# Performance work log

Hardware: AMD Instinct MI355X
Metric: run time of the kernel (lower is better)

Reference implementation:

```python
import jax, jax.numpy as jnp
import numpy as np

V, D, H, L, S, B, FF, MAXLEN = 50257, 768, 12, 12, 1024, 4, 3072, 1024
HD = D // H
EPS = 1e-5


def layernorm(x, w, b):
    m = jnp.mean(x, axis=-1, keepdims=True)
    v = jnp.mean(jnp.square(x - m), axis=-1, keepdims=True)
    return (x - m) * jax.lax.rsqrt(v + EPS) * w + b


def setup_inputs() -> dict:
    key = jax.random.key(0)
    ks = jax.random.split(key, 8)
    std = 0.02
    return {
        "tokens": jax.random.randint(ks[0], (B, S), 0, V, dtype=jnp.int32),
        "wte": std * jax.random.normal(ks[1], (V, D), jnp.float32),
        "wpe": std * jax.random.normal(ks[2], (1, MAXLEN, D), jnp.float32),
        "ln1_w": jnp.ones((L, D), jnp.float32),
        "ln1_b": jnp.zeros((L, D), jnp.float32),
        "ln2_w": jnp.ones((L, D), jnp.float32),
        "ln2_b": jnp.zeros((L, D), jnp.float32),
        "W_exp": std * jax.random.normal(ks[3], (L, D, 3 * D), jnp.float32),
        "b_exp": jnp.zeros((L, 3 * D), jnp.float32),
        "W_o": std * jax.random.normal(ks[4], (L, D, D), jnp.float32),
        "b_o": jnp.zeros((L, D), jnp.float32),
        "W_ff1": std * jax.random.normal(ks[5], (L, D, FF), jnp.float32),
        "b_ff1": jnp.zeros((L, FF), jnp.float32),
        "W_ff2": std * jax.random.normal(ks[6], (L, FF, D), jnp.float32),
        "b_ff2": jnp.zeros((L, D), jnp.float32),
    }


def reference(tokens, wte, wpe, ln1_w, ln1_b, ln2_w, ln2_b,
              W_exp, b_exp, W_o, b_o, W_ff1, b_ff1, W_ff2, b_ff2):
    Bc, Sc = tokens.shape
    x = wte[tokens] + wpe[:, :Sc, :]                      # [B,S,D]
    mask = jnp.tril(jnp.ones((Sc, Sc), bool))             # causal (past=None)
    scale = 1.0 / jnp.sqrt(jnp.float32(HD))
    presents = []
    for l in range(L):
        h = layernorm(x, ln1_w[l], ln1_b[l])
        qkv = h @ W_exp[l] + b_exp[l]                     # [B,S,3D]
        q, k, v = jnp.split(qkv, 3, axis=-1)
        q = q.reshape(Bc, Sc, H, HD)
        k = k.reshape(Bc, Sc, H, HD)
        v = v.reshape(Bc, Sc, H, HD)
        presents.append(jnp.stack([k, v]))                # [2,B,S,H,HD]
        score = jnp.einsum('bqhd,bkhd->bhqk', q, k)
        score = jnp.where(mask, score, jnp.float32(-1e20))
        attn = jax.nn.softmax(score * scale, axis=-1)     # mask applied BEFORE scaling, as in source
        a = jnp.einsum('bhqk,bkhd->bqhd', attn, v).reshape(Bc, Sc, D)
        a = a @ W_o[l] + b_o[l]
        add = layernorm(a + x, ln2_w[l], ln2_b[l])        # LN2 on residual sum (GPT2-variant in source)
        ff = jax.nn.gelu(add @ W_ff1[l] + b_ff1[l], approximate=False)
        ff = ff @ W_ff2[l] + b_ff2[l]
        x = ff + add
    return x, jnp.stack(presents)                         # [L,2,B,S,H,HD]
```

## Files before the change

### kernel.cpp

```cpp
#include <hip/hip_runtime.h>
#include <hip/hip_bf16.h>
#include <math.h>

#define Bc 4
#define Sc 1024
#define Dc 768
#define Hc 12
#define Lc 12
#define FFc 3072
#define Mtot (Bc*Sc)

typedef __bf16 bf16x8 __attribute__((ext_vector_type(8)));
typedef float f32x4 __attribute__((ext_vector_type(4)));

__device__ __forceinline__ void gload_lds16(const void* g, void* l) {
    __builtin_amdgcn_global_load_lds((const __attribute__((address_space(1))) void*)g,
                                     (__attribute__((address_space(3))) void*)l, 16, 0, 0);
}

template <int N>
__device__ __forceinline__ void waitcnt_vm() {
    if constexpr (N == 0)       asm volatile("s_waitcnt vmcnt(0)" ::: "memory");
    else if constexpr (N == 4)  asm volatile("s_waitcnt vmcnt(4)" ::: "memory");
    else if constexpr (N == 5)  asm volatile("s_waitcnt vmcnt(5)" ::: "memory");
    else if constexpr (N == 8)  asm volatile("s_waitcnt vmcnt(8)" ::: "memory");
    else if constexpr (N == 10) asm volatile("s_waitcnt vmcnt(10)" ::: "memory");
    else static_assert(N == 0, "unsupported vmcnt");
}

__global__ __launch_bounds__(256) void embed_kernel(const int* __restrict__ tokens,
                                                    const float* __restrict__ wte,
                                                    const float* __restrict__ wpe,
                                                    float* __restrict__ x) {
    int row = blockIdx.x;
    int s = row & (Sc - 1);
    int tok = tokens[row];
    const float* wt = wte + (size_t)tok * Dc;
    const float* wp = wpe + (size_t)s * Dc;
    float* xr = x + (size_t)row * Dc;
#pragma unroll
    for (int k = 0; k < 3; ++k) {
        int d = threadIdx.x + k * 256;
        xr[d] = wt[d] + wp[d];
    }
}

__global__ __launch_bounds__(256) void prep_kernel(
        const float* __restrict__ We, const float* __restrict__ Wo,
        const float* __restrict__ Wf1, const float* __restrict__ Wf2,
        __bf16* __restrict__ Te, __bf16* __restrict__ To,
        __bf16* __restrict__ Tf1, __bf16* __restrict__ Tf2,
        const float* __restrict__ x, const float* __restrict__ lw,
        const float* __restrict__ lb, __bf16* __restrict__ outb) {
    __shared__ float shm[32 * 33];
    int bid = blockIdx.x;
    if (bid < 6912) {
        const float* W; __bf16* T; int K, N, t;
        if (bid < 1728)      { W = We;  T = Te;  K = 768;  N = 2304; t = bid; }
        else if (bid < 2304) { W = Wo;  T = To;  K = 768;  N = 768;  t = bid - 1728; }
        else if (bid < 4608) { W = Wf1; T = Tf1; K = 768;  N = 3072; t = bid - 2304; }
        else                 { W = Wf2; T = Tf2; K = 3072; N = 768;  t = bid - 4608; }
        int nx = N >> 5;
        int n0 = (t % nx) * 32, k0 = (t / nx) * 32;
        int tx = threadIdx.x & 31, ty = threadIdx.x >> 5;
#pragma unroll
        for (int i = 0; i < 4; ++i)
            shm[(ty + 8 * i) * 33 + tx] = W[(size_t)(k0 + ty + 8 * i) * N + n0 + tx];
        __syncthreads();
#pragma unroll
        for (int i = 0; i < 4; ++i)
            T[(size_t)(n0 + ty + 8 * i) * K + k0 + tx] = (__bf16)shm[tx * 33 + ty + 8 * i];
    } else {
        int row = bid - 6912;
        const float* xr = x + (size_t)row * Dc;
        int t = threadIdx.x;
        float v0 = xr[t], v1 = xr[t + 256], v2 = xr[t + 512];
        float s1 = v0 + v1 + v2;
        float s2 = v0 * v0 + v1 * v1 + v2 * v2;
#pragma unroll
        for (int o = 32; o; o >>= 1) {
            s1 += __shfl_down(s1, o);
            s2 += __shfl_down(s2, o);
        }
        int wv = t >> 6;
        if ((t & 63) == 0) { shm[wv] = s1; shm[4 + wv] = s2; }
        __syncthreads();
        float S1 = shm[0] + shm[1] + shm[2] + shm[3];
        float S2 = shm[4] + shm[5] + shm[6] + shm[7];
        float mean = S1 * (1.0f / Dc);
        float var = S2 * (1.0f / Dc) - mean * mean;
        float rs = rsqrtf(var + 1e-5f);
        size_t ro = (size_t)row * Dc;
        outb[ro + t]       = (__bf16)((v0 - mean) * rs * lw[t]       + lb[t]);
        outb[ro + t + 256] = (__bf16)((v1 - mean) * rs * lw[t + 256] + lb[t + 256]);
        outb[ro + t + 512] = (__bf16)((v2 - mean) * rs * lw[t + 512] + lb[t + 512]);
    }
}

__global__ __launch_bounds__(256) void ln_kernel(const float* __restrict__ x,
                                                 const float* __restrict__ lw,
                                                 const float* __restrict__ lb,
                                                 __bf16* __restrict__ outb,
                                                 float* __restrict__ outf) {
    int row = blockIdx.x;
    const float* xr = x + (size_t)row * Dc;
    int t = threadIdx.x;
    float v0 = xr[t], v1 = xr[t + 256], v2 = xr[t + 512];
    float s1 = v0 + v1 + v2;
    float s2 = v0 * v0 + v1 * v1 + v2 * v2;
    __shared__ float red[8];
#pragma unroll
    for (int o = 32; o; o >>= 1) {
        s1 += __shfl_down(s1, o);
        s2 += __shfl_down(s2, o);
    }
    int wv = t >> 6;
    if ((t & 63) == 0) { red[wv] = s1; red[4 + wv] = s2; }
    __syncthreads();
    float S1 = red[0] + red[1] + red[2] + red[3];
    float S2 = red[4] + red[5] + red[6] + red[7];
    float mean = S1 * (1.0f / Dc);
    float var = S2 * (1.0f / Dc) - mean * mean;
    float rs = rsqrtf(var + 1e-5f);
    size_t ro = (size_t)row * Dc;
    float o0 = (v0 - mean) * rs * lw[t]       + lb[t];
    float o1 = (v1 - mean) * rs * lw[t + 256] + lb[t + 256];
    float o2 = (v2 - mean) * rs * lw[t + 512] + lb[t + 512];
    outb[ro + t]       = (__bf16)o0;
    outb[ro + t + 256] = (__bf16)o1;
    outb[ro + t + 512] = (__bf16)o2;
    outf[ro + t]       = o0;
    outf[ro + t + 256] = o1;
    outf[ro + t + 512] = o2;
}

template <int BMr, int BNc, int BK, int EPI>
__global__ __launch_bounds__(256) void gemm_bf16(const __bf16* __restrict__ A,
                                                 const __bf16* __restrict__ BT,
                                                 const float* __restrict__ bias,
                                                 const float* __restrict__ addin,
                                                 float* __restrict__ Cf,
                                                 __bf16* __restrict__ Cb,
                                                 float* __restrict__ pres,
                                                 int K, int N) {
    constexpr int HRm = BMr / 32, HRn = BNc / 32;
    constexpr int KS  = BK / 32;
    constexpr int LPR = BK / 8;
    constexpr int SSH = (BK == 32) ? 1 : 0;
    constexpr int IA  = BMr * BK / 2048;
    constexpr int IB  = BNc * BK / 2048;
    constexpr int S1w = IA + IB;
    static_assert(IA * 2048 == BMr * BK && IB * 2048 == BNc * BK, "staging granularity");
    __shared__ __bf16 As[3][BMr * BK];
    __shared__ __bf16 Bs[3][BNc * BK];
    int tid = threadIdx.x;
    int w = tid >> 6, l = tid & 63;
    int wrow = (w >> 1) * (BMr / 2), wcol = (w & 1) * (BNc / 2);
    int brow0 = blockIdx.x * BMr, bcol0 = blockIdx.y * BNc;
    int rsel = l & 15, lg = l >> 4;

    f32x4 acc[HRm][HRn] = {};

    const __bf16* Abase = A + (size_t)brow0 * K;
    const __bf16* Bbase = BT + (size_t)bcol0 * K;

    auto stage = [&](int buf, int kt) {
#pragma unroll
        for (int i = 0; i < IA; ++i) {
            int cid = i * 256 + tid;
            int row = cid / LPR, slot = cid % LPR;
            int chunk = slot ^ ((row >> SSH) & (LPR - 1));
            gload_lds16(Abase + (size_t)row * K + kt + chunk * 8,
                        &As[buf][(i * 256 + w * 64) * 8]);
        }
#pragma unroll
        for (int i = 0; i < IB; ++i) {
            int cid = i * 256 + tid;
            int row = cid / LPR, slot = cid % LPR;
            int chunk = slot ^ ((row >> SSH) & (LPR - 1));
            gload_lds16(Bbase + (size_t)row * K + kt + chunk * 8,
                        &Bs[buf][(i * 256 + w * 64) * 8]);
        }
    };

    int nk = K / BK;
    stage(0, 0);
    stage(1, BK);
    int cur = 0;
    for (int kt = 0; kt < nk; ++kt) {
        if (kt + 2 < nk) {
            int b2 = cur + 2; if (b2 >= 3) b2 -= 3;
            stage(b2, (kt + 2) * BK);
            waitcnt_vm<2 * S1w>();
        } else if (kt + 1 < nk) {
            waitcnt_vm<S1w>();
        } else {
            waitcnt_vm<0>();
        }
        __builtin_amdgcn_s_barrier();
        __builtin_amdgcn_sched_barrier(0);

        bf16x8 af[KS][HRm], bfr[KS][HRn];
#pragma unroll
        for (int m = 0; m < HRm; ++m) {
            int r = wrow + m * 16 + rsel;
            int sw = (r >> SSH) & (LPR - 1);
#pragma unroll
            for (int s = 0; s < KS; ++s)
                af[s][m] = *(const bf16x8*)(&As[cur][r * BK + ((s * 4 + lg) ^ sw) * 8]);
        }
#pragma unroll
        for (int n = 0; n < HRn; ++n) {
            int r = wcol + n * 16 + rsel;
            int sw = (r >> SSH) & (LPR - 1);
#pragma unroll
            for (int s = 0; s < KS; ++s)
                bfr[s][n] = *(const bf16x8*)(&Bs[cur][r * BK + ((s * 4 + lg) ^ sw) * 8]);
        }
#pragma unroll
        for (int s = 0; s < KS; ++s)
#pragma unroll
            for (int m = 0; m < HRm; ++m)
#pragma unroll
                for (int n = 0; n < HRn; ++n)
                    acc[m][n] = __builtin_amdgcn_mfma_f32_16x16x32_bf16(af[s][m], bfr[s][n], acc[m][n], 0, 0, 0);

        __builtin_amdgcn_sched_barrier(0);
        __builtin_amdgcn_s_barrier();
        cur = (cur == 2) ? 0 : cur + 1;
    }

    int r4 = lg * 4, cc = rsel;
#pragma unroll
    for (int m = 0; m < HRm; ++m)
#pragma unroll
        for (int n = 0; n < HRn; ++n) {
            int col = bcol0 + wcol + n * 16 + cc;
            float bv = bias[col];
#pragma unroll
            for (int i = 0; i < 4; ++i) {
                int row = brow0 + wrow + m * 16 + r4 + i;
                float v = acc[m][n][i] + bv;
                if (EPI == 1) {
                    v += addin[(size_t)row * N + col];
                    Cf[(size_t)row * N + col] = v;
                }
                if (EPI == 2) {
                    float u = 0.7978845608f * (v + 0.044715f * v * v * v);
                    v = v / (1.0f + __expf(-2.0f * u));
                    Cb[(size_t)row * N + col] = (__bf16)v;
                }
                if (EPI == 3) {
                    Cb[(size_t)row * N + col] = (__bf16)v;
                    if (col >= 768) {
                        int kv = (col >= 1536) ? 1 : 0;
                        pres[((size_t)kv * Mtot + row) * Dc + (col - 768 - kv * 768)] = v;
                    }
                }
            }
        }
}

__global__ __launch_bounds__(256) void attn_mfma_kernel(const __bf16* __restrict__ qkvb,
                                                        __bf16* __restrict__ aout) {
    __shared__ __bf16 Ks[64 * 72];
    __shared__ __bf16 Vts[64 * 72];
    __shared__ __bf16 Ps[4][16 * 72];
    int bh = blockIdx.x;
    int b = bh / Hc, h = bh % Hc;
    int qt = (Sc / 64 - 1) - blockIdx.y;
    int tid = threadIdx.x;
    int w = tid >> 6, l = tid & 63;
    int lr = l & 15, lg = l >> 4;
    int qb = qt * 64;

    const __bf16* base = qkvb + (size_t)b * Sc * 2304 + h * 64;

    bf16x8 qf[2];
    {
        const __bf16* qrow = base + (size_t)(qb + w * 16 + lr) * 2304 + lg * 8;
        qf[0] = *(const bf16x8*)(qrow);
        qf[1] = *(const bf16x8*)(qrow + 32);
    }

    f32x4 O[4] = {};
    float mrow[4], lrowv[4];
#pragma unroll
    for (int i = 0; i < 4; ++i) { mrow[i] = -1e30f; lrowv[i] = 0.0f; }

    int kj = tid >> 2, kc = tid & 3;
    int vj = tid & 63, vd0 = (tid >> 6) * 8;

    for (int t = 0; t <= qt; ++t) {
        __syncthreads();
#pragma unroll
        for (int it = 0; it < 2; ++it) {
            int c = kc + 4 * it;
            bf16x8 v = *(const bf16x8*)(base + (size_t)(t * 64 + kj) * 2304 + 768 + c * 8);
            *(bf16x8*)(&Ks[kj * 72 + c * 8]) = v;
        }
#pragma unroll
        for (int it = 0; it < 2; ++it) {
            int d0 = vd0 + 32 * it;
            bf16x8 v = *(const bf16x8*)(base + (size_t)(t * 64 + vj) * 2304 + 1536 + d0);
#pragma unroll
            for (int i = 0; i < 8; ++i)
                Vts[(d0 + i) * 72 + vj] = v[i];
        }
        __syncthreads();

        f32x4 sc[4] = {};
        __builtin_amdgcn_s_setprio(1);
#pragma unroll
        for (int s = 0; s < 2; ++s)
#pragma unroll
            for (int n = 0; n < 4; ++n) {
                bf16x8 kf = *(const bf16x8*)(&Ks[(n * 16 + lr) * 72 + s * 32 + lg * 8]);
                sc[n] = __builtin_amdgcn_mfma_f32_16x16x32_bf16(qf[s], kf, sc[n], 0, 0, 0);
            }
        __builtin_amdgcn_s_setprio(0);

        bool diag = (t == qt);
#pragma unroll
        for (int n = 0; n < 4; ++n)
#pragma unroll
            for (int i = 0; i < 4; ++i) {
                float s = sc[n][i] * 0.125f;
                if (diag) {
                    int jg = n * 16 + lr;
                    int qg = w * 16 + lg * 4 + i;
                    if (jg > qg) s = -1e30f;
                }
                sc[n][i] = s;
            }
        float corr[4], psum[4];
#pragma unroll
        for (int i = 0; i < 4; ++i) {
            float mx = fmaxf(fmaxf(sc[0][i], sc[1][i]), fmaxf(sc[2][i], sc[3][i]));
#pragma unroll
            for (int o = 1; o < 16; o <<= 1) mx = fmaxf(mx, __shfl_xor(mx, o));
            float mnew = fmaxf(mrow[i], mx);
            corr[i] = __expf(mrow[i] - mnew);
            mrow[i] = mnew;
            psum[i] = 0.0f;
        }
#pragma unroll
        for (int n = 0; n < 4; ++n)
#pragma unroll
            for (int i = 0; i < 4; ++i) {
                float p = __expf(sc[n][i] - mrow[i]);
                psum[i] += p;
                Ps[w][(lg * 4 + i) * 72 + n * 16 + lr] = (__bf16)p;
            }
#pragma unroll
        for (int i = 0; i < 4; ++i) {
#pragma unroll
            for (int o = 1; o < 16; o <<= 1) psum[i] += __shfl_xor(psum[i], o);
            lrowv[i] = lrowv[i] * corr[i] + psum[i];
        }
#pragma unroll
        for (int n = 0; n < 4; ++n)
#pragma unroll
            for (int i = 0; i < 4; ++i) O[n][i] *= corr[i];
        __builtin_amdgcn_s_setprio(1);
#pragma unroll
        for (int s = 0; s < 2; ++s) {
            bf16x8 pf = *(const bf16x8*)(&Ps[w][lr * 72 + s * 32 + lg * 8]);
#pragma unroll
            for (int n = 0; n < 4; ++n) {
                bf16x8 vf = *(const bf16x8*)(&Vts[(n * 16 + lr) * 72 + s * 32 + lg * 8]);
                O[n] = __builtin_amdgcn_mfma_f32_16x16x32_bf16(pf, vf, O[n], 0, 0, 0);
            }
        }
        __builtin_amdgcn_s_setprio(0);
    }
    __bf16* orow = aout + (size_t)(b * Sc + qb + w * 16 + lg * 4) * Dc + h * 64 + lr;
#pragma unroll
    for (int n = 0; n < 4; ++n)
#pragma unroll
        for (int i = 0; i < 4; ++i)
            orow[(size_t)i * Dc + n * 16] = (__bf16)(O[n][i] / lrowv[i]);
}

extern "C" void kernel_launch(void* const* d_in, const int* in_sizes, int n_in,
                              void* d_out, int out_size, void* d_ws, size_t ws_size,
                              hipStream_t stream) {
    const int*   tokens = (const int*)d_in[0];
    const float* wte    = (const float*)d_in[1];
    const float* wpe    = (const float*)d_in[2];
    const float* ln1_w  = (const float*)d_in[3];
    const float* ln1_b  = (const float*)d_in[4];
    const float* ln2_w  = (const float*)d_in[5];
    const float* ln2_b  = (const float*)d_in[6];
    const float* W_exp  = (const float*)d_in[7];
    const float* b_exp  = (const float*)d_in[8];
    const float* W_o    = (const float*)d_in[9];
    const float* b_o    = (const float*)d_in[10];
    const float* W_ff1  = (const float*)d_in[11];
    const float* b_ff1  = (const float*)d_in[12];
    const float* W_ff2  = (const float*)d_in[13];
    const float* b_ff2  = (const float*)d_in[14];

    float* out_x    = (float*)d_out;
    float* out_pres = out_x + (size_t)Mtot * Dc;

    float* ws   = (float*)d_ws;
    float* x    = ws;
    float* addf = x + (size_t)Mtot * Dc;
    __bf16* hb   = (__bf16*)(addf + (size_t)Mtot * Dc);
    __bf16* addb = hb + (size_t)Mtot * Dc;
    __bf16* qkvb = addb + (size_t)Mtot * Dc;
    __bf16* ff1b = qkvb + (size_t)Mtot * 3 * Dc;
    __bf16* wt_exp = ff1b + (size_t)Mtot * FFc;
    __bf16* wt_o   = wt_exp + (size_t)2304 * 768;
    __bf16* wt_ff1 = wt_o   + (size_t)768 * 768;
    __bf16* wt_ff2 = wt_ff1 + (size_t)3072 * 768;

    embed_kernel<<<Mtot, 256, 0, stream>>>(tokens, wte, wpe, x);

    for (int lidx = 0; lidx < Lc; ++lidx) {
        prep_kernel<<<6912 + Mtot, 256, 0, stream>>>(
            W_exp + (size_t)lidx * 768 * 2304, W_o + (size_t)lidx * 768 * 768,
            W_ff1 + (size_t)lidx * 768 * 3072, W_ff2 + (size_t)lidx * 3072 * 768,
            wt_exp, wt_o, wt_ff1, wt_ff2,
            x, ln1_w + lidx * Dc, ln1_b + lidx * Dc, hb);

        gemm_bf16<64, 192, 32, 3><<<dim3(Mtot / 64, 2304 / 192), 256, 0, stream>>>(
            hb, wt_exp, b_exp + (size_t)lidx * 3 * Dc,
            nullptr, nullptr, qkvb, out_pres + (size_t)lidx * 2 * Mtot * Dc, 768, 2304);
        attn_mfma_kernel<<<dim3(Bc * Hc, Sc / 64), 256, 0, stream>>>(qkvb, hb);
        gemm_bf16<64, 96, 64, 1><<<dim3(Mtot / 64, 768 / 96), 256, 0, stream>>>(
            hb, wt_o, b_o + (size_t)lidx * Dc,
            x, x, nullptr, nullptr, 768, 768);
        ln_kernel<<<Mtot, 256, 0, stream>>>(
            x, ln2_w + lidx * Dc, ln2_b + lidx * Dc, addb, addf);
        gemm_bf16<128, 128, 32, 2><<<dim3(Mtot / 128, FFc / 128), 256, 0, stream>>>(
            addb, wt_ff1, b_ff1 + (size_t)lidx * FFc,
            nullptr, nullptr, ff1b, nullptr, 768, FFc);
        float* ff2dst = (lidx == Lc - 1) ? out_x : x;
        gemm_bf16<64, 96, 64, 1><<<dim3(Mtot / 64, 768 / 96), 256, 0, stream>>>(
            ff1b, wt_ff2, b_ff2 + (size_t)lidx * Dc,
            addf, ff2dst, nullptr, nullptr, 3072, 768);
    }
}
```

Baseline: 2.032 ms.

## Split-K the two N=768 GEMMs and fold partial sums into LayerNorm kernels

The attention-output and FF2 GEMMs now run as two K halves over a z grid dimension. One half adds bias and the residual; the other writes raw partial sums to a scratch buffer. The following LayerNorm kernels (ln2 and the next layer's prep) add the two partials, and a finalize kernel does the same for the output. This doubles the block count of these small-N GEMMs to improve CU occupancy and uses double buffering there. The cost is an extra fp32 write and read of the partial activations per GEMM, plus one extra kernel.

```diff
diff --git a/kernel.cpp b/kernel.cpp
--- a/kernel.cpp
+++ b/kernel.cpp
@@ -45,13 +45,16 @@
     }
 }
 
+template <bool SUMIN>
 __global__ __launch_bounds__(256) void prep_kernel(
         const float* __restrict__ We, const float* __restrict__ Wo,
         const float* __restrict__ Wf1, const float* __restrict__ Wf2,
         __bf16* __restrict__ Te, __bf16* __restrict__ To,
         __bf16* __restrict__ Tf1, __bf16* __restrict__ Tf2,
-        const float* __restrict__ x, const float* __restrict__ lw,
-        const float* __restrict__ lb, __bf16* __restrict__ outb) {
+        const float* __restrict__ xin0, const float* __restrict__ xin1,
+        float* __restrict__ xout,
+        const float* __restrict__ lw, const float* __restrict__ lb,
+        __bf16* __restrict__ outb) {
     __shared__ float shm[32 * 33];
     int bid = blockIdx.x;
     if (bid < 6912) {
@@ -72,9 +75,17 @@
             T[(size_t)(n0 + ty + 8 * i) * K + k0 + tx] = (__bf16)shm[tx * 33 + ty + 8 * i];
     } else {
         int row = bid - 6912;
-        const float* xr = x + (size_t)row * Dc;
+        size_t ro = (size_t)row * Dc;
         int t = threadIdx.x;
-        float v0 = xr[t], v1 = xr[t + 256], v2 = xr[t + 512];
+        float v0, v1, v2;
+        if (SUMIN) {
+            v0 = xin0[ro + t]       + xin1[ro + t];
+            v1 = xin0[ro + t + 256] + xin1[ro + t + 256];
+            v2 = xin0[ro + t + 512] + xin1[ro + t + 512];
+            xout[ro + t] = v0; xout[ro + t + 256] = v1; xout[ro + t + 512] = v2;
+        } else {
+            v0 = xin0[ro + t]; v1 = xin0[ro + t + 256]; v2 = xin0[ro + t + 512];
+        }
         float s1 = v0 + v1 + v2;
         float s2 = v0 * v0 + v1 * v1 + v2 * v2;
 #pragma unroll
@@ -90,22 +101,24 @@
         float mean = S1 * (1.0f / Dc);
         float var = S2 * (1.0f / Dc) - mean * mean;
         float rs = rsqrtf(var + 1e-5f);
-        size_t ro = (size_t)row * Dc;
         outb[ro + t]       = (__bf16)((v0 - mean) * rs * lw[t]       + lb[t]);
         outb[ro + t + 256] = (__bf16)((v1 - mean) * rs * lw[t + 256] + lb[t + 256]);
         outb[ro + t + 512] = (__bf16)((v2 - mean) * rs * lw[t + 512] + lb[t + 512]);
     }
 }
 
-__global__ __launch_bounds__(256) void ln_kernel(const float* __restrict__ x,
-                                                 const float* __restrict__ lw,
-                                                 const float* __restrict__ lb,
-                                                 __bf16* __restrict__ outb,
-                                                 float* __restrict__ outf) {
+__global__ __launch_bounds__(256) void ln2_kernel(const float* __restrict__ xin0,
+                                                  const float* __restrict__ xin1,
+                                                  const float* __restrict__ lw,
+                                                  const float* __restrict__ lb,
+                                                  __bf16* __restrict__ outb,
+                                                  float* __restrict__ outf) {
     int row = blockIdx.x;
-    const float* xr = x + (size_t)row * Dc;
+    size_t ro = (size_t)row * Dc;
     int t = threadIdx.x;
-    float v0 = xr[t], v1 = xr[t + 256], v2 = xr[t + 512];
+    float v0 = xin0[ro + t]       + xin1[ro + t];
+    float v1 = xin0[ro + t + 256] + xin1[ro + t + 256];
+    float v2 = xin0[ro + t + 512] + xin1[ro + t + 512];
     float s1 = v0 + v1 + v2;
     float s2 = v0 * v0 + v1 * v1 + v2 * v2;
     __shared__ float red[8];
@@ -122,7 +135,6 @@
     float mean = S1 * (1.0f / Dc);
     float var = S2 * (1.0f / Dc) - mean * mean;
     float rs = rsqrtf(var + 1e-5f);
-    size_t ro = (size_t)row * Dc;
     float o0 = (v0 - mean) * rs * lw[t]       + lb[t];
     float o1 = (v1 - mean) * rs * lw[t + 256] + lb[t + 256];
     float o2 = (v2 - mean) * rs * lw[t + 512] + lb[t + 512];
@@ -134,15 +146,26 @@
     outf[ro + t + 512] = o2;
 }
 
-template <int BMr, int BNc, int BK, int EPI>
+__global__ __launch_bounds__(256) void finalize_kernel(const float* __restrict__ a,
+                                                       const float* __restrict__ b,
+                                                       float* __restrict__ out) {
+    size_t idx = ((size_t)blockIdx.x * 256 + threadIdx.x) * 4;
+    float4 va = *(const float4*)(a + idx);
+    float4 vb = *(const float4*)(b + idx);
+    float4 o = make_float4(va.x + vb.x, va.y + vb.y, va.z + vb.z, va.w + vb.w);
+    *(float4*)(out + idx) = o;
+}
+
+template <int BMr, int BNc, int BK, int EPI, int NBUF, bool SPLIT>
 __global__ __launch_bounds__(256) void gemm_bf16(const __bf16* __restrict__ A,
                                                  const __bf16* __restrict__ BT,
                                                  const float* __restrict__ bias,
                                                  const float* __restrict__ addin,
                                                  float* __restrict__ Cf,
+                                                 float* __restrict__ Cf2,
                                                  __bf16* __restrict__ Cb,
                                                  float* __restrict__ pres,
-                                                 int K, int N) {
+                                                 int K, int Kst, int N) {
     constexpr int HRm = BMr / 32, HRn = BNc / 32;
     constexpr int KS  = BK / 32;
     constexpr int LPR = BK / 8;
@@ -151,18 +174,19 @@
     constexpr int IB  = BNc * BK / 2048;
     constexpr int S1w = IA + IB;
     static_assert(IA * 2048 == BMr * BK && IB * 2048 == BNc * BK, "staging granularity");
-    __shared__ __bf16 As[3][BMr * BK];
-    __shared__ __bf16 Bs[3][BNc * BK];
+    __shared__ __bf16 As[NBUF][BMr * BK];
+    __shared__ __bf16 Bs[NBUF][BNc * BK];
     int tid = threadIdx.x;
     int w = tid >> 6, l = tid & 63;
     int wrow = (w >> 1) * (BMr / 2), wcol = (w & 1) * (BNc / 2);
     int brow0 = blockIdx.x * BMr, bcol0 = blockIdx.y * BNc;
+    int koff = SPLIT ? blockIdx.z * K : 0;
     int rsel = l & 15, lg = l >> 4;
 
     f32x4 acc[HRm][HRn] = {};
 
-    const __bf16* Abase = A + (size_t)brow0 * K;
-    const __bf16* Bbase = BT + (size_t)bcol0 * K;
+    const __bf16* Abase = A + (size_t)brow0 * Kst + koff;
+    const __bf16* Bbase = BT + (size_t)bcol0 * Kst + koff;
 
     auto stage = [&](int buf, int kt) {
 #pragma unroll
@@ -170,7 +194,7 @@
             int cid = i * 256 + tid;
             int row = cid / LPR, slot = cid % LPR;
             int chunk = slot ^ ((row >> SSH) & (LPR - 1));
-            gload_lds16(Abase + (size_t)row * K + kt + chunk * 8,
+            gload_lds16(Abase + (size_t)row * Kst + kt + chunk * 8,
                         &As[buf][(i * 256 + w * 64) * 8]);
         }
 #pragma unroll
@@ -178,24 +202,33 @@
             int cid = i * 256 + tid;
             int row = cid / LPR, slot = cid % LPR;
             int chunk = slot ^ ((row >> SSH) & (LPR - 1));
-            gload_lds16(Bbase + (size_t)row * K + kt + chunk * 8,
+            gload_lds16(Bbase + (size_t)row * Kst + kt + chunk * 8,
                         &Bs[buf][(i * 256 + w * 64) * 8]);
         }
     };
 
     int nk = K / BK;
     stage(0, 0);
-    stage(1, BK);
+    if (NBUF == 3) stage(1, BK);
     int cur = 0;
     for (int kt = 0; kt < nk; ++kt) {
-        if (kt + 2 < nk) {
-            int b2 = cur + 2; if (b2 >= 3) b2 -= 3;
-            stage(b2, (kt + 2) * BK);
-            waitcnt_vm<2 * S1w>();
-        } else if (kt + 1 < nk) {
-            waitcnt_vm<S1w>();
+        if (NBUF == 3) {
+            if (kt + 2 < nk) {
+                int b2 = cur + 2; if (b2 >= 3) b2 -= 3;
+                stage(b2, (kt + 2) * BK);
+                waitcnt_vm<2 * S1w>();
+            } else if (kt + 1 < nk) {
+                waitcnt_vm<S1w>();
+            } else {
+                waitcnt_vm<0>();
+            }
         } else {
-            waitcnt_vm<0>();
+            if (kt + 1 < nk) {
+                stage(cur ^ 1, (kt + 1) * BK);
+                waitcnt_vm<S1w>();
+            } else {
+                waitcnt_vm<0>();
+            }
         }
         __builtin_amdgcn_s_barrier();
         __builtin_amdgcn_sched_barrier(0);
@@ -227,20 +260,26 @@
 
         __builtin_amdgcn_sched_barrier(0);
         __builtin_amdgcn_s_barrier();
-        cur = (cur == 2) ? 0 : cur + 1;
+        if (NBUF == 3) { cur = (cur == 2) ? 0 : cur + 1; } else { cur ^= 1; }
     }
 
     int r4 = lg * 4, cc = rsel;
+    bool rawpart = SPLIT && (blockIdx.z == 1);
 #pragma unroll
     for (int m = 0; m < HRm; ++m)
 #pragma unroll
         for (int n = 0; n < HRn; ++n) {
             int col = bcol0 + wcol + n * 16 + cc;
-            float bv = bias[col];
+            float bv = rawpart ? 0.0f : bias[col];
 #pragma unroll
             for (int i = 0; i < 4; ++i) {
                 int row = brow0 + wrow + m * 16 + r4 + i;
-                float v = acc[m][n][i] + bv;
+                float v = acc[m][n][i];
+                if (rawpart) {
+                    Cf2[(size_t)row * N + col] = v;
+                    continue;
+                }
+                v += bv;
                 if (EPI == 1) {
                     v += addin[(size_t)row * N + col];
                     Cf[(size_t)row * N + col] = v;
@@ -407,7 +446,9 @@
     float* ws   = (float*)d_ws;
     float* x    = ws;
     float* addf = x + (size_t)Mtot * Dc;
-    __bf16* hb   = (__bf16*)(addf + (size_t)Mtot * Dc);
+    float* p1w  = addf + (size_t)Mtot * Dc;
+    float* q1   = p1w + (size_t)Mtot * Dc;
+    __bf16* hb   = (__bf16*)(q1 + (size_t)Mtot * Dc);
     __bf16* addb = hb + (size_t)Mtot * Dc;
     __bf16* qkvb = addb + (size_t)Mtot * Dc;
     __bf16* ff1b = qkvb + (size_t)Mtot * 3 * Dc;
@@ -419,27 +460,35 @@
     embed_kernel<<<Mtot, 256, 0, stream>>>(tokens, wte, wpe, x);
 
     for (int lidx = 0; lidx < Lc; ++lidx) {
-        prep_kernel<<<6912 + Mtot, 256, 0, stream>>>(
-            W_exp + (size_t)lidx * 768 * 2304, W_o + (size_t)lidx * 768 * 768,
-            W_ff1 + (size_t)lidx * 768 * 3072, W_ff2 + (size_t)lidx * 3072 * 768,
-            wt_exp, wt_o, wt_ff1, wt_ff2,
-            x, ln1_w + lidx * Dc, ln1_b + lidx * Dc, hb);
-
-        gemm_bf16<64, 192, 32, 3><<<dim3(Mtot / 64, 2304 / 192), 256, 0, stream>>>(
+        if (lidx == 0) {
+            prep_kernel<false><<<6912 + Mtot, 256, 0, stream>>>(
+                W_exp, W_o, W_ff1, W_ff2, wt_exp, wt_o, wt_ff1, wt_ff2,
+                x, nullptr, nullptr, ln1_w, ln1_b, hb);
+        } else {
+            prep_kernel<true><<<6912 + Mtot, 256, 0, stream>>>(
+                W_exp + (size_t)lidx * 768 * 2304, W_o + (size_t)lidx * 768 * 768,
+                W_ff1 + (size_t)lidx * 768 * 3072, W_ff2 + (size_t)lidx * 3072 * 768,
+                wt_exp, wt_o, wt_ff1, wt_ff2,
+                addf, q1, x, ln1_w + lidx * Dc, ln1_b + lidx * Dc, hb);
+        }
+
+        gemm_bf16<64, 192, 32, 3, 3, false><<<dim3(Mtot / 64, 2304 / 192), 256, 0, stream>>>(
             hb, wt_exp, b_exp + (size_t)lidx * 3 * Dc,
-            nullptr, nullptr, qkvb, out_pres + (size_t)lidx * 2 * Mtot * Dc, 768, 2304);
+            nullptr, nullptr, nullptr, qkvb,
+            out_pres + (size_t)lidx * 2 * Mtot * Dc, 768, 768, 2304);
         attn_mfma_kernel<<<dim3(Bc * Hc, Sc / 64), 256, 0, stream>>>(qkvb, hb);
-        gemm_bf16<64, 96, 64, 1><<<dim3(Mtot / 64, 768 / 96), 256, 0, stream>>>(
+        gemm_bf16<64, 96, 64, 1, 2, true><<<dim3(Mtot / 64, 768 / 96, 2), 256, 0, stream>>>(
             hb, wt_o, b_o + (size_t)lidx * Dc,
-            x, x, nullptr, nullptr, 768, 768);
-        ln_kernel<<<Mtot, 256, 0, stream>>>(
-            x, ln2_w + lidx * Dc, ln2_b + lidx * Dc, addb, addf);
-        gemm_bf16<128, 128, 32, 2><<<dim3(Mtot / 128, FFc / 128), 256, 0, stream>>>(
+            x, x, p1w, nullptr, nullptr, 384, 768, 768);
+        ln2_kernel<<<Mtot, 256, 0, stream>>>(
+            x, p1w, ln2_w + lidx * Dc, ln2_b + lidx * Dc, addb, addf);
+        gemm_bf16<128, 128, 32, 2, 3, false><<<dim3(Mtot / 128, FFc / 128), 256, 0, stream>>>(
             addb, wt_ff1, b_ff1 + (size_t)lidx * FFc,
-            nullptr, nullptr, ff1b, nullptr, 768, FFc);
-        float* ff2dst = (lidx == Lc - 1) ? out_x : x;
-        gemm_bf16<64, 96, 64, 1><<<dim3(Mtot / 64, 768 / 96), 256, 0, stream>>>(
+            nullptr, nullptr, nullptr, ff1b, nullptr, 768, 768, FFc);
+        gemm_bf16<64, 96, 64, 1, 2, true><<<dim3(Mtot / 64, 768 / 96, 2), 256, 0, stream>>>(
             ff1b, wt_ff2, b_ff2 + (size_t)lidx * Dc,
-            addf, ff2dst, nullptr, nullptr, 3072, 768);
-    }
-}
+            addf, addf, q1, nullptr, nullptr, 1536, 3072, 768);
+    }
+
+    finalize_kernel<<<(Mtot * Dc) / 1024, 256, 0, stream>>>(addf, q1, out_x);
+}
```

Result: no change. 2.068 ms (+1.8%).
